# Kernel tuning notes

Hardware: AMD Instinct MI355X
Metric: run time of the kernel (lower is better)

The kernel has to match this reference:

```python
import jax, jax.numpy as jnp
import numpy as np

B, P, ENC = 64, 196, 2048
E, H, A, V, T = 512, 512, 512, 10000, 20


def setup_inputs() -> dict:
    key = jax.random.key(0)
    ks = jax.random.split(key, 20)
    s = 0.02
    return {
        "img_feat": jax.random.normal(ks[0], (B, P, ENC), jnp.float32),
        "captions": jax.random.randint(ks[1], (B, T), 0, V),
        "embedding": jax.random.normal(ks[2], (V, E)) * s,
        "W_enc_att": jax.random.normal(ks[3], (A, ENC)) * s,
        "b_enc_att": jnp.zeros((A,)),
        "W_dec_att": jax.random.normal(ks[4], (A, H)) * s,
        "b_dec_att": jnp.zeros((A,)),
        "W_full": jax.random.normal(ks[5], (1, A)) * s,
        "b_full": jnp.zeros((1,)),
        "W_beta": jax.random.normal(ks[6], (ENC, H)) * s,
        "b_beta": jnp.zeros((ENC,)),
        "W_ih": jax.random.normal(ks[7], (4 * H, E + ENC)) * s,
        "b_ih": jnp.zeros((4 * H,)),
        "W_hh": jax.random.normal(ks[8], (4 * H, H)) * s,
        "b_hh": jnp.zeros((4 * H,)),
        "W_init_h": jax.random.normal(ks[9], (H, ENC)) * s,
        "b_init_h": jnp.zeros((H,)),
        "W_init_c": jax.random.normal(ks[10], (H, ENC)) * s,
        "b_init_c": jnp.zeros((H,)),
        "W_out": jax.random.normal(ks[11], (V, H)) * s,
        "b_out": jnp.zeros((V,)),
    }


def reference(img_feat, captions, embedding,
              W_enc_att, b_enc_att, W_dec_att, b_dec_att, W_full, b_full,
              W_beta, b_beta, W_ih, b_ih, W_hh, b_hh,
              W_init_h, b_init_h, W_init_c, b_init_c, W_out, b_out):
    # init hidden from mean image feature
    avg = img_feat.mean(axis=1)                              # [B, ENC]
    h = avg @ W_init_h.T + b_init_h                          # [B, H]
    c = avg @ W_init_c.T + b_init_c

    # encoder-side attention projection is timestep-invariant
    enc_proj = jnp.einsum('bpe,ae->bpa', img_feat, W_enc_att) + b_enc_att  # [B,P,A]

    emb = embedding[captions]                                # [B, T, E]
    emb_t = jnp.swapaxes(emb, 0, 1)                          # [T, B, E]
    Hd = h.shape[-1]

    def step(carry, e_t):
        h, c = carry
        # additive attention
        dec = h @ W_dec_att.T + b_dec_att                    # [B, A]
        att = jnp.einsum('bpa,a->bp', enc_proj + dec[:, None, :], W_full[0]) + b_full[0]
        alpha = jax.nn.softmax(att, axis=1)                  # [B, P]
        context = jnp.einsum('bpe,bp->be', img_feat, alpha)  # [B, ENC]
        # gate
        gate = jax.nn.sigmoid(h @ W_beta.T + b_beta)         # [B, ENC]
        x = jnp.concatenate([e_t, gate * context], axis=1)   # [B, E+ENC]
        # LSTM cell
        gates = x @ W_ih.T + b_ih + h @ W_hh.T + b_hh        # [B, 4H]
        i, f, g, o = jnp.split(gates, 4, axis=1)
        c_new = jax.nn.sigmoid(f) * c + jax.nn.sigmoid(i) * jnp.tanh(g)
        h_new = jax.nn.sigmoid(o) * jnp.tanh(c_new)
        pred = h_new @ W_out.T + b_out                       # [B, V]
        return (h_new, c_new), (pred, alpha)

    (_, _), (preds, alphas) = jax.lax.scan(step, (h, c), emb_t)
    preds = jnp.swapaxes(preds, 0, 1)    # [B, T, V]
    alphas = jnp.swapaxes(alphas, 0, 1)  # [B, T, P]
    return preds, alphas
```

## Files before the change

### kernel.cpp

```cpp
#include <hip/hip_runtime.h>
#include <math.h>

#define Bsz 64
#define Pp  196
#define ENC 2048
#define Ee  512
#define Hh  512
#define Vv  10000
#define Tt  20
#define H4  2048

typedef short bf16x8 __attribute__((ext_vector_type(8)));
typedef float f32x4 __attribute__((ext_vector_type(4)));

__device__ __forceinline__ float sigmoidf_(float x) { return 1.0f / (1.0f + expf(-x)); }

__device__ __forceinline__ unsigned short bf16r(float x) {
    union { float f; unsigned int u; } c; c.f = x;
    unsigned int lsb = (c.u >> 16) & 1u;
    return (unsigned short)((c.u + 0x7fffu + lsb) >> 16);
}

__global__ __launch_bounds__(256) void k_venc(const float* __restrict__ W_full,
                                              const float* __restrict__ W_enc,
                                              float* __restrict__ v_enc) {
    int lane = threadIdx.x & 63, ag = threadIdx.x >> 6;
    int e = blockIdx.x * 64 + lane;
    float s = 0.f;
    #pragma unroll 8
    for (int a = ag * 128; a < ag * 128 + 128; ++a)
        s += W_full[a] * W_enc[(size_t)a * ENC + e];
    __shared__ float red[4][64];
    red[ag][lane] = s;
    __syncthreads();
    if (threadIdx.x < 64)
        v_enc[e] = red[0][lane] + red[1][lane] + red[2][lane] + red[3][lane];
}

__global__ __launch_bounds__(256) void k_scores(const float* __restrict__ img,
                                                const float* __restrict__ v_enc,
                                                float* __restrict__ sc) {
    int b = blockIdx.y;
    int wave = threadIdx.x >> 6, lane = threadIdx.x & 63;
    int p = blockIdx.x * 4 + wave;
    __shared__ float4 sv[ENC / 4];
    const float4* ve4 = (const float4*)v_enc;
    sv[threadIdx.x] = ve4[threadIdx.x];
    sv[threadIdx.x + 256] = ve4[threadIdx.x + 256];
    __syncthreads();
    const float4* row = (const float4*)(img + ((size_t)b * Pp + p) * ENC);
    float s = 0.f;
    #pragma unroll
    for (int it = 0; it < 8; ++it) {
        int idx = it * 64 + lane;
        float4 v = row[idx];
        float4 w = sv[idx];
        s += v.x * w.x + v.y * w.y + v.z * w.z + v.w * w.w;
    }
    #pragma unroll
    for (int off = 32; off > 0; off >>= 1) s += __shfl_down(s, off);
    if (lane == 0) sc[b * Pp + p] = s;
}

__global__ __launch_bounds__(256) void k_softmax(const float* __restrict__ sc,
                                                 float* __restrict__ alpha,
                                                 float* __restrict__ alphas_out) {
    int b = blockIdx.x, tid = threadIdx.x;
    __shared__ float red[256];
    __shared__ float sa[Pp];
    float v = (tid < Pp) ? sc[b * Pp + tid] : -INFINITY;
    red[tid] = v; __syncthreads();
    for (int off = 128; off > 0; off >>= 1) {
        if (tid < off) red[tid] = fmaxf(red[tid], red[tid + off]);
        __syncthreads();
    }
    float mx = red[0]; __syncthreads();
    float ex = (tid < Pp) ? expf(v - mx) : 0.f;
    red[tid] = ex; __syncthreads();
    for (int off = 128; off > 0; off >>= 1) {
        if (tid < off) red[tid] += red[tid + off];
        __syncthreads();
    }
    float inv = 1.f / red[0];
    if (tid < Pp) { sa[tid] = ex * inv; alpha[b * Pp + tid] = ex * inv; }
    __syncthreads();
    for (int i = tid; i < Tt * Pp; i += 256)
        alphas_out[(size_t)b * Tt * Pp + i] = sa[i % Pp];
}

__global__ __launch_bounds__(256) void k_ctx(const float* __restrict__ img,
                                             const float* __restrict__ alpha,
                                             float* __restrict__ context,
                                             float* __restrict__ avg) {
    int b = blockIdx.y;
    int e2 = blockIdx.x * 256 + threadIdx.x;
    __shared__ float sa[Pp];
    if (threadIdx.x < Pp) sa[threadIdx.x] = alpha[b * Pp + threadIdx.x];
    __syncthreads();
    const float2* ib2 = (const float2*)(img + (size_t)b * Pp * ENC);
    float cx = 0.f, cy = 0.f, ax = 0.f, ay = 0.f;
    for (int p = 0; p < Pp; p += 4) {
        #pragma unroll
        for (int q = 0; q < 4; ++q) {
            float ap = sa[p + q];
            float2 v = ib2[(size_t)(p + q) * (ENC / 2) + e2];
            cx += ap * v.x; cy += ap * v.y;
            ax += v.x;      ay += v.y;
        }
    }
    float2* c2 = (float2*)(context + (size_t)b * ENC);
    float2* a2 = (float2*)(avg + (size_t)b * ENC);
    c2[e2] = make_float2(cx, cy);
    a2[e2] = make_float2(ax * (1.f / 196.f), ay * (1.f / 196.f));
}

template<int MODE>
__global__ __launch_bounds__(256) void gemm_step(
    const float* __restrict__ A,
    const float* __restrict__ B0, const float* __restrict__ B1,
    float* __restrict__ C, float* __restrict__ P,
    const float* __restrict__ bias0, const float* __restrict__ bias1,
    const float* __restrict__ extra) {
    const int tid = threadIdx.x;
    const int tx = tid & 15, ty = tid >> 4;
    const int n0 = blockIdx.x * 16;

    int lda, ldb, nch, kbase = 0;
    const float* Brow;
    if (MODE == 0) {
        lda = 2048; ldb = 2048; nch = 32;
        Brow = (n0 < 512) ? B0 + (size_t)n0 * 2048 : B1 + (size_t)(n0 - 512) * 2048;
    } else if (MODE == 1) {
        lda = 1024; ldb = 512; nch = 8;
        Brow = (n0 < 2048) ? B0 + (size_t)n0 * 512 : B1 + (size_t)(n0 - 2048) * 512;
    } else {
        lda = 2048; ldb = 2560; nch = 8; kbase = blockIdx.y * 512;
        Brow = B0 + (size_t)n0 * 2560 + 512 + kbase;
    }

    __shared__ float As[64][68];
    __shared__ float Bs[64][20];

    float4 pa[4], pb;
    const int sm[4] = { tid >> 4, (256 + tid) >> 4, (512 + tid) >> 4, (768 + tid) >> 4 };
    const int scc = tid & 15;
    const int bn = tid >> 4, bc = tid & 15;

    auto load_chunk = [&](int c) {
        int k0 = c * 64;
        #pragma unroll
        for (int i = 0; i < 4; ++i)
            pa[i] = *(const float4*)(A + (size_t)sm[i] * lda + kbase + k0 + 4 * scc);
        pb = *(const float4*)(Brow + (size_t)bn * ldb + k0 + 4 * bc);
    };

    float acc[4] = {};
    load_chunk(0);
    for (int c = 0; c < nch; ++c) {
        __syncthreads();
        #pragma unroll
        for (int i = 0; i < 4; ++i) {
            As[4 * scc + 0][sm[i]] = pa[i].x;
            As[4 * scc + 1][sm[i]] = pa[i].y;
            As[4 * scc + 2][sm[i]] = pa[i].z;
            As[4 * scc + 3][sm[i]] = pa[i].w;
        }
        Bs[4 * bc + 0][bn] = pb.x;
        Bs[4 * bc + 1][bn] = pb.y;
        Bs[4 * bc + 2][bn] = pb.z;
        Bs[4 * bc + 3][bn] = pb.w;
        __syncthreads();
        if (c + 1 < nch) load_chunk(c + 1);
        #pragma unroll 8
        for (int kk = 0; kk < 64; ++kk) {
            float4 a = *(const float4*)&As[kk][ty * 4];
            float bb = Bs[kk][tx];
            acc[0] += a.x * bb; acc[1] += a.y * bb;
            acc[2] += a.z * bb; acc[3] += a.w * bb;
        }
    }

    int gn = n0 + tx;
    #pragma unroll
    for (int i = 0; i < 4; ++i) {
        int m = ty * 4 + i;
        if (MODE == 0) {
            float bsel = (n0 < 512) ? bias0[gn] : bias1[gn - 512];
            C[(size_t)m * 1024 + gn] = acc[i] + bsel;
        } else if (MODE == 1) {
            if (n0 < 2048) {
                float s = sigmoidf_(acc[i] + bias0[gn]);
                C[(size_t)m * 2048 + gn] = s * extra[(size_t)m * 2048 + gn];
            } else {
                P[(size_t)m * 2048 + gn - 2048] = acc[i];
            }
        } else {
            P[(size_t)(blockIdx.y + 1) * (64 * 2048) + (size_t)m * 2048 + gn] = acc[i];
        }
    }
}

__global__ __launch_bounds__(256) void gemm_emb(const int* __restrict__ captions,
                                                const float* __restrict__ emb,
                                                const float* __restrict__ Bm,
                                                float* __restrict__ C,
                                                const float* __restrict__ bias,
                                                const float* __restrict__ bias2) {
    const int tid = threadIdx.x;
    const int tx = tid & 15, ty = tid >> 4;
    const int m0 = blockIdx.y * 128, n0 = blockIdx.x * 64;

    __shared__ float As[32][132];
    __shared__ float Bs[32][68];

    float4 pa[4], pb[2];
    const int am[4] = { tid >> 3, (256 + tid) >> 3, (512 + tid) >> 3, (768 + tid) >> 3 };
    const int ac = tid & 7;
    const int bnr[2] = { tid >> 3, (256 + tid) >> 3 };
    const int bc = tid & 7;

    const float* arow[4];
    #pragma unroll
    for (int i = 0; i < 4; ++i) {
        int r = m0 + am[i];
        arow[i] = emb + (size_t)captions[(r & 63) * Tt + (r >> 6)] * Ee;
    }

    const int nchunk = Ee / 32;
    auto load_chunk = [&](int c) {
        int k0 = c * 32;
        #pragma unroll
        for (int i = 0; i < 4; ++i)
            pa[i] = *(const float4*)(arow[i] + k0 + 4 * ac);
        #pragma unroll
        for (int i = 0; i < 2; ++i)
            pb[i] = *(const float4*)(Bm + (size_t)(n0 + bnr[i]) * 2560 + k0 + 4 * bc);
    };

    float acc[8][4] = {};
    load_chunk(0);
    for (int c = 0; c < nchunk; ++c) {
        __syncthreads();
        #pragma unroll
        for (int i = 0; i < 4; ++i) {
            As[4 * ac + 0][am[i]] = pa[i].x;
            As[4 * ac + 1][am[i]] = pa[i].y;
            As[4 * ac + 2][am[i]] = pa[i].z;
            As[4 * ac + 3][am[i]] = pa[i].w;
        }
        #pragma unroll
        for (int i = 0; i < 2; ++i) {
            Bs[4 * bc + 0][bnr[i]] = pb[i].x;
            Bs[4 * bc + 1][bnr[i]] = pb[i].y;
            Bs[4 * bc + 2][bnr[i]] = pb[i].z;
            Bs[4 * bc + 3][bnr[i]] = pb[i].w;
        }
        __syncthreads();
        if (c + 1 < nchunk) load_chunk(c + 1);
        #pragma unroll 4
        for (int kk = 0; kk < 32; ++kk) {
            float4 a0 = *(const float4*)&As[kk][ty * 8];
            float4 a1 = *(const float4*)&As[kk][ty * 8 + 4];
            float4 b0 = *(const float4*)&Bs[kk][tx * 4];
            float av[8] = { a0.x, a0.y, a0.z, a0.w, a1.x, a1.y, a1.z, a1.w };
            float bv[4] = { b0.x, b0.y, b0.z, b0.w };
            #pragma unroll
            for (int i = 0; i < 8; ++i)
                #pragma unroll
                for (int j = 0; j < 4; ++j)
                    acc[i][j] += av[i] * bv[j];
        }
    }

    #pragma unroll
    for (int i = 0; i < 8; ++i) {
        int m = m0 + ty * 8 + i;
        #pragma unroll
        for (int j = 0; j < 4; ++j) {
            int gn = n0 + tx * 4 + j;
            C[(size_t)m * H4 + gn] = acc[i][j] + bias[gn] + bias2[gn];
        }
    }
}

__global__ __launch_bounds__(256) void k_lstm(const float* __restrict__ ep,
                                              const float* __restrict__ P,
                                              float* __restrict__ hc,
                                              unsigned short* __restrict__ Hbf) {
    int idx = blockIdx.x * 256 + threadIdx.x;
    int b = idx >> 9, j = idx & 511;
    const float* e = ep + (size_t)b * 2048;
    const float* p0 = P + (size_t)b * 2048;
    const float* p1 = p0 + 64 * 2048;
    const float* p2 = p1 + 64 * 2048;
    const float* p3 = p2 + 64 * 2048;
    const float* p4 = p3 + 64 * 2048;
    auto gsum = [&](int col) {
        return e[col] + p0[col] + p1[col] + p2[col] + p3[col] + p4[col];
    };
    float i_ = sigmoidf_(gsum(j));
    float f_ = sigmoidf_(gsum(j + 512));
    float g_ = tanhf(gsum(j + 1024));
    float o_ = sigmoidf_(gsum(j + 1536));
    float* hrow = hc + (size_t)b * 1024;
    float cn = f_ * hrow[512 + j] + i_ * g_;
    float hn = o_ * tanhf(cn);
    hrow[512 + j] = cn;
    hrow[j] = hn;
    Hbf[(size_t)b * Hh + j] = bf16r(hn);
}

__global__ __launch_bounds__(256) void k_cvt(const float* __restrict__ src,
                                             unsigned short* __restrict__ dst) {
    int i = blockIdx.x * 256 + threadIdx.x;
    if (i >= (Vv * Hh) / 4) return;
    float4 v = ((const float4*)src)[i];
    ushort4 o;
    o.x = bf16r(v.x); o.y = bf16r(v.y); o.z = bf16r(v.z); o.w = bf16r(v.w);
    ((ushort4*)dst)[i] = o;
}

__global__ __launch_bounds__(256) void gemm_preds(const unsigned short* __restrict__ Hb,
                                                  const unsigned short* __restrict__ Wb,
                                                  const float* __restrict__ b_out,
                                                  float* __restrict__ preds) {
    const int tid = threadIdx.x;
    const int lane = tid & 63, wave = tid >> 6;
    const int wr = wave >> 1, wc = wave & 1;
    const int m0 = blockIdx.y * 128, n0 = blockIdx.x * 128;

    __shared__ unsigned short As[128][40];
    __shared__ unsigned short Bs[128][40];

    const int r0 = tid >> 2, c8 = (tid & 3) * 8;
    uint4 pa[2], pb[2];
    auto load = [&](int c) {
        int k0 = c * 32;
        #pragma unroll
        for (int i = 0; i < 2; ++i) {
            int r = r0 + i * 64;
            pa[i] = *(const uint4*)(Hb + (size_t)(m0 + r) * 512 + k0 + c8);
            int gn = n0 + r; gn = (gn > Vv - 1) ? (Vv - 1) : gn;
            pb[i] = *(const uint4*)(Wb + (size_t)gn * 512 + k0 + c8);
        }
    };

    union F8 { bf16x8 v; struct { unsigned long long lo, hi; } u; };
    f32x4 acc[4][4] = {};

    const int arow = wr * 64 + (lane & 15);
    const int brow = wc * 64 + (lane & 15);
    const int kg = (lane >> 4) * 4;

    load(0);
    for (int c = 0; c < 16; ++c) {
        __syncthreads();
        #pragma unroll
        for (int i = 0; i < 2; ++i) {
            *(uint4*)&As[r0 + i * 64][c8] = pa[i];
            *(uint4*)&Bs[r0 + i * 64][c8] = pb[i];
        }
        __syncthreads();
        if (c < 15) load(c + 1);
        F8 af[4], bfr[4];
        #pragma unroll
        for (int x = 0; x < 4; ++x) {
            af[x].u.lo  = *(const unsigned long long*)&As[arow + x * 16][kg];
            af[x].u.hi  = *(const unsigned long long*)&As[arow + x * 16][16 + kg];
            bfr[x].u.lo = *(const unsigned long long*)&Bs[brow + x * 16][kg];
            bfr[x].u.hi = *(const unsigned long long*)&Bs[brow + x * 16][16 + kg];
        }
        #pragma unroll
        for (int mi = 0; mi < 4; ++mi)
            #pragma unroll
            for (int ni = 0; ni < 4; ++ni)
                acc[mi][ni] = __builtin_amdgcn_mfma_f32_16x16x32_bf16(
                    af[mi].v, bfr[ni].v, acc[mi][ni], 0, 0, 0);
    }

    const int crow = (lane >> 4) * 4, ccol = lane & 15;
    #pragma unroll
    for (int mi = 0; mi < 4; ++mi) {
        #pragma unroll
        for (int ni = 0; ni < 4; ++ni) {
            int n = n0 + wc * 64 + ni * 16 + ccol;
            if (n >= Vv) continue;
            float bo = b_out[n];
            #pragma unroll
            for (int r = 0; r < 4; ++r) {
                int m = m0 + wr * 64 + mi * 16 + crow + r;
                int t = m >> 6, b = m & 63;
                preds[(size_t)(b * Tt + t) * Vv + n] = acc[mi][ni][r] + bo;
            }
        }
    }
}

extern "C" void kernel_launch(void* const* d_in, const int* in_sizes, int n_in,
                              void* d_out, int out_size, void* d_ws, size_t ws_size,
                              hipStream_t stream) {
    const float* img_feat  = (const float*)d_in[0];
    const int*   captions  = (const int*)d_in[1];
    const float* embedding = (const float*)d_in[2];
    const float* W_enc_att = (const float*)d_in[3];
    const float* W_full    = (const float*)d_in[7];
    const float* W_beta    = (const float*)d_in[9];
    const float* b_beta    = (const float*)d_in[10];
    const float* W_ih      = (const float*)d_in[11];
    const float* b_ih      = (const float*)d_in[12];
    const float* W_hh      = (const float*)d_in[13];
    const float* b_hh      = (const float*)d_in[14];
    const float* W_init_h  = (const float*)d_in[15];
    const float* b_init_h  = (const float*)d_in[16];
    const float* W_init_c  = (const float*)d_in[17];
    const float* b_init_c  = (const float*)d_in[18];
    const float* W_out     = (const float*)d_in[19];
    const float* b_out     = (const float*)d_in[20];

    float* preds_out  = (float*)d_out;
    float* alphas_out = (float*)d_out + (size_t)Bsz * Tt * Vv;

    float* ws = (float*)d_ws;
    float* v_enc    = ws;
    float* sc       = v_enc + ENC;
    float* alpha    = sc + Bsz * Pp;
    float* context  = alpha + Bsz * Pp;
    float* avg      = context + Bsz * ENC;
    float* hc       = avg + Bsz * ENC;
    float* gc       = hc + Bsz * 1024;
    float* Pbuf     = gc + Bsz * ENC;
    float* emb_part = Pbuf + 5 * Bsz * H4;
    unsigned short* H_bf16 = (unsigned short*)(emb_part + (size_t)Tt * Bsz * H4);
    unsigned short* Wout_bf16 = (unsigned short*)emb_part;

    k_venc<<<32, 256, 0, stream>>>(W_full, W_enc_att, v_enc);
    k_scores<<<dim3(49, 64), 256, 0, stream>>>(img_feat, v_enc, sc);
    k_softmax<<<64, 256, 0, stream>>>(sc, alpha, alphas_out);
    k_ctx<<<dim3(4, 64), 256, 0, stream>>>(img_feat, alpha, context, avg);

    gemm_step<0><<<64, 256, 0, stream>>>(
        avg, W_init_h, W_init_c, hc, nullptr, b_init_h, b_init_c, nullptr);

    gemm_emb<<<dim3(H4 / 64, (Tt * Bsz) / 128), 256, 0, stream>>>(
        captions, embedding, W_ih, emb_part, b_ih, b_hh);

    for (int t = 0; t < Tt; ++t) {
        gemm_step<1><<<256, 256, 0, stream>>>(
            hc, W_beta, W_hh, gc, Pbuf, b_beta, nullptr, context);
        gemm_step<2><<<dim3(128, 4), 256, 0, stream>>>(
            gc, W_ih, nullptr, nullptr, Pbuf, nullptr, nullptr, nullptr);
        k_lstm<<<128, 256, 0, stream>>>(
            emb_part + (size_t)t * Bsz * H4, Pbuf, hc,
            H_bf16 + (size_t)t * Bsz * Hh);
    }

    k_cvt<<<(Vv * Hh / 4 + 255) / 256, 256, 0, stream>>>(W_out, Wout_bf16);

    gemm_preds<<<dim3((Vv + 127) / 128, (Tt * Bsz) / 128), 256, 0, stream>>>(
        H_bf16, Wout_bf16, b_out, preds_out);
}
```

Before: 1.505 ms.

## Fuse recurrent LSTM time loop into one persistent cooperative kernel

Replaces the 60 per-timestep launches (two small GEMMs plus an LSTM pointwise kernel per step) with a single cooperative kernel that loops over all timesteps and uses grid-wide syncs between the gate projection and the LSTM update. Each thread computes dot products directly from global memory with per-thread weight rows and double-buffered h, removing launch overhead and the split-K partial-sum buffer. H is written in batch-major order so the output GEMM stores preds contiguously, and that GEMM's grid axes are swapped. The risks are grid.sync cost, reliance on all 256 blocks being co-resident, and uncoalesced, untiled weight reads in the fused loop.

New measurement: 5.825 ms. 287% more time.

```diff
diff --git a/kernel.cpp b/kernel.cpp
--- a/kernel.cpp
+++ b/kernel.cpp
@@ -1,5 +1,8 @@
 #include <hip/hip_runtime.h>
+#include <hip/hip_cooperative_groups.h>
 #include <math.h>
+
+namespace cg = cooperative_groups;
 
 #define Bsz 64
 #define Pp  196
@@ -114,29 +117,16 @@
     a2[e2] = make_float2(ax * (1.f / 196.f), ay * (1.f / 196.f));
 }
 
-template<int MODE>
-__global__ __launch_bounds__(256) void gemm_step(
+__global__ __launch_bounds__(256) void gemm_init(
     const float* __restrict__ A,
     const float* __restrict__ B0, const float* __restrict__ B1,
-    float* __restrict__ C, float* __restrict__ P,
-    const float* __restrict__ bias0, const float* __restrict__ bias1,
-    const float* __restrict__ extra) {
+    float* __restrict__ h0, float* __restrict__ cbuf,
+    const float* __restrict__ bias0, const float* __restrict__ bias1) {
     const int tid = threadIdx.x;
     const int tx = tid & 15, ty = tid >> 4;
     const int n0 = blockIdx.x * 16;
 
-    int lda, ldb, nch, kbase = 0;
-    const float* Brow;
-    if (MODE == 0) {
-        lda = 2048; ldb = 2048; nch = 32;
-        Brow = (n0 < 512) ? B0 + (size_t)n0 * 2048 : B1 + (size_t)(n0 - 512) * 2048;
-    } else if (MODE == 1) {
-        lda = 1024; ldb = 512; nch = 8;
-        Brow = (n0 < 2048) ? B0 + (size_t)n0 * 512 : B1 + (size_t)(n0 - 2048) * 512;
-    } else {
-        lda = 2048; ldb = 2560; nch = 8; kbase = blockIdx.y * 512;
-        Brow = B0 + (size_t)n0 * 2560 + 512 + kbase;
-    }
+    const float* Brow = (n0 < 512) ? B0 + (size_t)n0 * ENC : B1 + (size_t)(n0 - 512) * ENC;
 
     __shared__ float As[64][68];
     __shared__ float Bs[64][20];
@@ -150,13 +140,13 @@
         int k0 = c * 64;
         #pragma unroll
         for (int i = 0; i < 4; ++i)
-            pa[i] = *(const float4*)(A + (size_t)sm[i] * lda + kbase + k0 + 4 * scc);
-        pb = *(const float4*)(Brow + (size_t)bn * ldb + k0 + 4 * bc);
+            pa[i] = *(const float4*)(A + (size_t)sm[i] * ENC + k0 + 4 * scc);
+        pb = *(const float4*)(Brow + (size_t)bn * ENC + k0 + 4 * bc);
     };
 
     float acc[4] = {};
     load_chunk(0);
-    for (int c = 0; c < nch; ++c) {
+    for (int c = 0; c < 32; ++c) {
         __syncthreads();
         #pragma unroll
         for (int i = 0; i < 4; ++i) {
@@ -170,7 +160,7 @@
         Bs[4 * bc + 2][bn] = pb.z;
         Bs[4 * bc + 3][bn] = pb.w;
         __syncthreads();
-        if (c + 1 < nch) load_chunk(c + 1);
+        if (c + 1 < 32) load_chunk(c + 1);
         #pragma unroll 8
         for (int kk = 0; kk < 64; ++kk) {
             float4 a = *(const float4*)&As[kk][ty * 4];
@@ -184,19 +174,8 @@
     #pragma unroll
     for (int i = 0; i < 4; ++i) {
         int m = ty * 4 + i;
-        if (MODE == 0) {
-            float bsel = (n0 < 512) ? bias0[gn] : bias1[gn - 512];
-            C[(size_t)m * 1024 + gn] = acc[i] + bsel;
-        } else if (MODE == 1) {
-            if (n0 < 2048) {
-                float s = sigmoidf_(acc[i] + bias0[gn]);
-                C[(size_t)m * 2048 + gn] = s * extra[(size_t)m * 2048 + gn];
-            } else {
-                P[(size_t)m * 2048 + gn - 2048] = acc[i];
-            }
-        } else {
-            P[(size_t)(blockIdx.y + 1) * (64 * 2048) + (size_t)m * 2048 + gn] = acc[i];
-        }
+        if (gn < 512) h0[(size_t)m * 512 + gn]           = acc[i] + bias0[gn];
+        else          cbuf[(size_t)m * 512 + (gn - 512)] = acc[i] + bias1[gn - 512];
     }
 }
 
@@ -283,31 +262,91 @@
     }
 }
 
-__global__ __launch_bounds__(256) void k_lstm(const float* __restrict__ ep,
-                                              const float* __restrict__ P,
-                                              float* __restrict__ hc,
-                                              unsigned short* __restrict__ Hbf) {
-    int idx = blockIdx.x * 256 + threadIdx.x;
-    int b = idx >> 9, j = idx & 511;
-    const float* e = ep + (size_t)b * 2048;
-    const float* p0 = P + (size_t)b * 2048;
-    const float* p1 = p0 + 64 * 2048;
-    const float* p2 = p1 + 64 * 2048;
-    const float* p3 = p2 + 64 * 2048;
-    const float* p4 = p3 + 64 * 2048;
-    auto gsum = [&](int col) {
-        return e[col] + p0[col] + p1[col] + p2[col] + p3[col] + p4[col];
-    };
-    float i_ = sigmoidf_(gsum(j));
-    float f_ = sigmoidf_(gsum(j + 512));
-    float g_ = tanhf(gsum(j + 1024));
-    float o_ = sigmoidf_(gsum(j + 1536));
-    float* hrow = hc + (size_t)b * 1024;
-    float cn = f_ * hrow[512 + j] + i_ * g_;
-    float hn = o_ * tanhf(cn);
-    hrow[512 + j] = cn;
-    hrow[j] = hn;
-    Hbf[(size_t)b * Hh + j] = bf16r(hn);
+__global__ __launch_bounds__(512) void k_loop(
+    const float* __restrict__ W_beta, const float* __restrict__ b_beta,
+    const float* __restrict__ W_ih,   const float* __restrict__ W_hh,
+    const float* __restrict__ context, const float* __restrict__ emb_part,
+    float* __restrict__ h0, float* __restrict__ h1,
+    float* __restrict__ cbuf, float* __restrict__ gc,
+    unsigned short* __restrict__ Hbf) {
+    cg::grid_group grid = cg::this_grid();
+    const int tid = threadIdx.x;
+    const int bid = blockIdx.x;
+    const int cgp = bid >> 2;
+    const int bg  = bid & 3;
+    const int local = tid & 31;
+    const int b = bg * 16 + (tid >> 5);
+
+    const int nA = cgp * 32 + local;
+    const float bbeta = b_beta[nA];
+    const float* wbrow = W_beta + (size_t)nA * 512;
+
+    const int gidx = local >> 3, jl = local & 7;
+    const int jB = cgp * 8 + jl;
+    const int G = gidx * 512 + jB;
+    const float* wgrow = W_ih + (size_t)G * 2560 + 512;
+    const float* whrow = W_hh + (size_t)G * 512;
+
+    float* hs[2] = { h0, h1 };
+
+    for (int t = 0; t < Tt; ++t) {
+        const float* h = hs[t & 1];
+        float* hn = hs[(t + 1) & 1];
+
+        {
+            const float4* hr = (const float4*)(h + (size_t)b * 512);
+            const float4* wr = (const float4*)wbrow;
+            float a0 = 0.f, a1 = 0.f, a2 = 0.f, a3 = 0.f;
+            #pragma unroll 8
+            for (int k = 0; k < 128; ++k) {
+                float4 hv = hr[k], wv = wr[k];
+                a0 += hv.x * wv.x; a1 += hv.y * wv.y;
+                a2 += hv.z * wv.z; a3 += hv.w * wv.w;
+            }
+            float s = sigmoidf_((a0 + a1) + (a2 + a3) + bbeta);
+            gc[(size_t)b * 2048 + nA] = s * context[(size_t)b * 2048 + nA];
+        }
+        grid.sync();
+
+        {
+            const float4* gr = (const float4*)(gc + (size_t)b * 2048);
+            const float4* wr = (const float4*)wgrow;
+            float a0 = 0.f, a1 = 0.f, a2 = 0.f, a3 = 0.f;
+            #pragma unroll 8
+            for (int k = 0; k < 512; ++k) {
+                float4 g = gr[k], w = wr[k];
+                a0 += g.x * w.x; a1 += g.y * w.y;
+                a2 += g.z * w.z; a3 += g.w * w.w;
+            }
+            const float4* hr = (const float4*)(h + (size_t)b * 512);
+            const float4* wh = (const float4*)whrow;
+            #pragma unroll 8
+            for (int k = 0; k < 128; ++k) {
+                float4 hv = hr[k], w = wh[k];
+                a0 += hv.x * w.x; a1 += hv.y * w.y;
+                a2 += hv.z * w.z; a3 += hv.w * w.w;
+            }
+            float v = (a0 + a1) + (a2 + a3)
+                    + emb_part[((size_t)t * 64 + b) * 2048 + G];
+            int lane = tid & 63;
+            float vf = __shfl(v, lane + 8);
+            float vg = __shfl(v, lane + 16);
+            float vo = __shfl(v, lane + 24);
+            if (gidx == 0) {
+                float i_ = sigmoidf_(v);
+                float f_ = sigmoidf_(vf);
+                float g_ = tanhf(vg);
+                float o_ = sigmoidf_(vo);
+                size_t ci = (size_t)b * 512 + jB;
+                float cn = f_ * cbuf[ci] + i_ * g_;
+                float hv2 = o_ * tanhf(cn);
+                cbuf[ci] = cn;
+                hn[ci] = hv2;
+                Hbf[((size_t)b * Tt + t) * 512 + jB] = bf16r(hv2);
+            }
+        }
+        grid.sync();
+    }
 }
 
 __global__ __launch_bounds__(256) void k_cvt(const float* __restrict__ src,
@@ -327,7 +366,7 @@
     const int tid = threadIdx.x;
     const int lane = tid & 63, wave = tid >> 6;
     const int wr = wave >> 1, wc = wave & 1;
-    const int m0 = blockIdx.y * 128, n0 = blockIdx.x * 128;
+    const int m0 = blockIdx.x * 128, n0 = blockIdx.y * 128;
 
     __shared__ unsigned short As[128][40];
     __shared__ unsigned short Bs[128][40];
@@ -389,8 +428,7 @@
             #pragma unroll
             for (int r = 0; r < 4; ++r) {
                 int m = m0 + wr * 64 + mi * 16 + crow + r;
-                int t = m >> 6, b = m & 63;
-                preds[(size_t)(b * Tt + t) * Vv + n] = acc[mi][ni][r] + bo;
+                preds[(size_t)m * Vv + n] = acc[mi][ni][r] + bo;
             }
         }
     }
@@ -426,10 +464,11 @@
     float* alpha    = sc + Bsz * Pp;
     float* context  = alpha + Bsz * Pp;
     float* avg      = context + Bsz * ENC;
-    float* hc       = avg + Bsz * ENC;
-    float* gc       = hc + Bsz * 1024;
-    float* Pbuf     = gc + Bsz * ENC;
-    float* emb_part = Pbuf + 5 * Bsz * H4;
+    float* h0buf    = avg + Bsz * ENC;
+    float* h1buf    = h0buf + Bsz * Hh;
+    float* cbuf     = h1buf + Bsz * Hh;
+    float* gc       = cbuf + Bsz * Hh;
+    float* emb_part = gc + Bsz * ENC;
     unsigned short* H_bf16 = (unsigned short*)(emb_part + (size_t)Tt * Bsz * H4);
     unsigned short* Wout_bf16 = (unsigned short*)emb_part;
 
@@ -438,24 +477,26 @@
     k_softmax<<<64, 256, 0, stream>>>(sc, alpha, alphas_out);
     k_ctx<<<dim3(4, 64), 256, 0, stream>>>(img_feat, alpha, context, avg);
 
-    gemm_step<0><<<64, 256, 0, stream>>>(
-        avg, W_init_h, W_init_c, hc, nullptr, b_init_h, b_init_c, nullptr);
+    gemm_init<<<64, 256, 0, stream>>>(
+        avg, W_init_h, W_init_c, h0buf, cbuf, b_init_h, b_init_c);
 
     gemm_emb<<<dim3(H4 / 64, (Tt * Bsz) / 128), 256, 0, stream>>>(
         captions, embedding, W_ih, emb_part, b_ih, b_hh);
 
-    for (int t = 0; t < Tt; ++t) {
-        gemm_step<1><<<256, 256, 0, stream>>>(
-            hc, W_beta, W_hh, gc, Pbuf, b_beta, nullptr, context);
-        gemm_step<2><<<dim3(128, 4), 256, 0, stream>>>(
-            gc, W_ih, nullptr, nullptr, Pbuf, nullptr, nullptr, nullptr);
-        k_lstm<<<128, 256, 0, stream>>>(
-            emb_part + (size_t)t * Bsz * H4, Pbuf, hc,
-            H_bf16 + (size_t)t * Bsz * Hh);
+    {
+        const float* a0 = W_beta;  const float* a1 = b_beta;
+        const float* a2 = W_ih;    const float* a3 = W_hh;
+        const float* a4 = context; const float* a5 = emb_part;
+        float* a6 = h0buf; float* a7 = h1buf;
+        float* a8 = cbuf;  float* a9 = gc;
+        unsigned short* a10 = H_bf16;
+        void* args[] = { &a0, &a1, &a2, &a3, &a4, &a5, &a6, &a7, &a8, &a9, &a10 };
+        hipLaunchCooperativeKernel((const void*)k_loop, dim3(256), dim3(512),
+                                   args, 0, stream);
     }
 
     k_cvt<<<(Vv * Hh / 4 + 255) / 256, 256, 0, stream>>>(W_out, Wout_bf16);
 
-    gemm_preds<<<dim3((Vv + 127) / 128, (Tt * Bsz) / 128), 256, 0, stream>>>(
+    gemm_preds<<<dim3((Tt * Bsz) / 128, (Vv + 127) / 128), 256, 0, stream>>>(
         H_bf16, Wout_bf16, b_out, preds_out);
 }
```
